# Performance work log

Measured on AMD Instinct MI355X. Metric: run time of the kernel, lower is better.

## Reference

```python
import jax, jax.numpy as jnp
import numpy as np


def setup_inputs() -> dict:
    key = jax.random.key(0)
    k1, k2, k3, k4, k5 = jax.random.split(key, 5)
    b, n, L, D, m = 8, 8192, 512, 128, 16
    x = jax.random.normal(k1, (b, n, L), dtype=jnp.float32)
    # attention MLP: Linear(L->D, no bias), Tanh, Linear(D->1, no bias)
    W1 = jax.random.normal(k2, (L, D), dtype=jnp.float32) / np.sqrt(L).astype(np.float32)
    W2 = jax.random.normal(k3, (D, 1), dtype=jnp.float32) / np.sqrt(D).astype(np.float32)
    batched_image_ids = jax.random.randint(k4, (b, n), 0, m)  # which image each packed token belongs to
    key_pad_mask = jax.random.bernoulli(k5, 0.1, (b, n))      # True = padding token
    return {"x": x, "W1": W1, "W2": W2,
            "batched_image_ids": batched_image_ids,
            "key_pad_mask": key_pad_mask,
            "max_queries": 16}


def reference(x, W1, W2, batched_image_ids, key_pad_mask, max_queries):
    # Attention scores per token: tanh(x W1) W2 -> [b, n, 1]
    A = jnp.tanh(x @ W1) @ W2
    A = jnp.swapaxes(A, -1, -2)  # [b, 1, n]
    b, n, d = x.shape
    # Per-image pooling mask: token j contributes to query i iff its image id == i and not padded
    image_id_arange = jnp.arange(max_queries)                                    # [m]
    attn_pool_mask = (image_id_arange[None, :, None] == batched_image_ids[:, None, :])
    attn_pool_mask = attn_pool_mask & (~key_pad_mask)[:, None, :]                # [b, m, n]
    neg = -jnp.finfo(A.dtype).max
    A = jnp.where(attn_pool_mask, jnp.broadcast_to(A, (b, max_queries, n)), neg)
    A = jax.nn.softmax(A, axis=-1)                                               # [b, m, n]
    out = jnp.einsum('bmn,bnd->bmd', A, x)                                       # pooled per image
    # num_images == max_queries for every bag -> is_images selects everything
    out = out.reshape(b * max_queries, d)
    return out
```

## Files before the change

### kernel.cpp

```cpp
#include <hip/hip_runtime.h>
#include <hip/hip_bf16.h>
#include <cstdint>
#include <cstddef>

typedef __attribute__((ext_vector_type(8))) short bf16x8;
typedef __attribute__((ext_vector_type(4))) float f32x4;

#define BATCH 8
#define NTOK 8192
#define LDIM 512
#define DDIM 128
#define NQ 16

static __device__ __forceinline__ short f2bf(float f) {
  uint32_t u = __float_as_uint(f);
  uint32_t r = u + 0x7fffu + ((u >> 16) & 1u);
  return (short)(r >> 16);
}

static __device__ __forceinline__ bf16x8 cvt8(float4 a, float4 b) {
  union { uint32_t u[4]; bf16x8 v; } r;
  asm("v_cvt_pk_bf16_f32 %0, %1, %2" : "=v"(r.u[0]) : "v"(a.x), "v"(a.y));
  asm("v_cvt_pk_bf16_f32 %0, %1, %2" : "=v"(r.u[1]) : "v"(a.z), "v"(a.w));
  asm("v_cvt_pk_bf16_f32 %0, %1, %2" : "=v"(r.u[2]) : "v"(b.x), "v"(b.y));
  asm("v_cvt_pk_bf16_f32 %0, %1, %2" : "=v"(r.u[3]) : "v"(b.z), "v"(b.w));
  return r.v;
}

static __device__ __forceinline__ uint32_t cvt2(float a, float b) {
  uint32_t o;
  asm("v_cvt_pk_bf16_f32 %0, %1, %2" : "=v"(o) : "v"(a), "v"(b));
  return o;
}

static __device__ __forceinline__ bool is_pad(const void* pad, int byteFlag, int j) {
  return byteFlag ? (((const unsigned char*)pad)[j] != 0)
                  : (((const int*)pad)[j] != 0);
}

__global__ __launch_bounds__(256) void k0_wfrag(const float* __restrict__ W1,
                                                short* __restrict__ wfrag,
                                                const unsigned int* __restrict__ pad_raw,
                                                int* __restrict__ flag) {
  int tid = blockIdx.x * blockDim.x + threadIdx.x;
  if (tid < 16 * 8 * 64) {
    int l = tid & 63;
    int t = (tid >> 6) & 7;
    int c = tid >> 9;
    int kbase = c * 32 + (l >> 4) * 8;
    int col = t * 16 + (l & 15);
    bf16x8 frag;
#pragma unroll
    for (int i = 0; i < 8; ++i) frag[i] = f2bf(W1[(size_t)(kbase + i) * DDIM + col]);
    ((bf16x8*)wfrag)[tid] = frag;
  }
  if (blockIdx.x == 0) {
    int any_gt1 = 0;
    for (int i = threadIdx.x; i < 16384; i += 256)
      if (pad_raw[i] > 1u) any_gt1 = 1;
    unsigned long long m = __ballot(any_gt1);
    __shared__ int s[4];
    if ((threadIdx.x & 63) == 0) s[threadIdx.x >> 6] = (m != 0ull) ? 1 : 0;
    __syncthreads();
    if (threadIdx.x == 0) flag[0] = (s[0] | s[1] | s[2] | s[3]);
  }
}

__global__ __launch_bounds__(256, 2) void k1_fused(const float* __restrict__ x,
                                                   const short* __restrict__ wfrag,
                                                   const float* __restrict__ W2,
                                                   const int* __restrict__ ids,
                                                   const void* __restrict__ pad,
                                                   const int* __restrict__ flag,
                                                   unsigned int* __restrict__ partial_bf,
                                                   float* __restrict__ wsum_p) {
  __shared__ __align__(16) char smem[81920];
  char* slab = smem;
  short* ldsW = (short*)(smem + 65536);
  float* wt_l = (float*)(smem + 65536);
  int* qq_l = (int*)(smem + 65536 + 256);
  int* idx_l = (int*)(smem + 65536 + 512);
  int* off_l = (int*)(smem + 65536 + 768);

  const int tid = threadIdx.x, wave = tid >> 6, lane = tid & 63;
  const int g = lane >> 4;
  const int row = wave * 16 + (lane & 15);
  const int rowB = blockIdx.x * 64;
  const float* xp = x + (size_t)(rowB + row) * LDIM + g * 8;
  const int swz = (row & 7) << 4;

#define STAGE_W(c, wb)                                                                        \
  {                                                                                           \
    const unsigned int* srcw_ = (const unsigned int*)wfrag + (c) * 2048;                      \
    _Pragma("unroll")                                                                         \
    for (int i = 0; i < 2; ++i) {                                                             \
      int off_ = i * 256 + tid;                                                               \
      __builtin_amdgcn_global_load_lds(                                                       \
          (const __attribute__((address_space(1))) unsigned int*)(srcw_ + off_ * 4),          \
          (__attribute__((address_space(3))) unsigned int*)&ldsW[(wb) * 4096 + off_ * 8],     \
          16, 0, 0);                                                                          \
    }                                                                                         \
  }

#define ALOAD(dst, c)                              \
  {                                                \
    dst[0] = *(const float4*)(xp + (c) * 32);      \
    dst[1] = *(const float4*)(xp + (c) * 32 + 4);  \
  }

  f32x4 acc[8];
#pragma unroll
  for (int t = 0; t < 8; ++t) acc[t] = (f32x4){0.f, 0.f, 0.f, 0.f};
  float4 avbuf[2][2];

  STAGE_W(0, 0);
  ALOAD(avbuf[0], 0);
  __syncthreads();

#pragma unroll
  for (int c = 0; c < 16; ++c) {
    if (c < 15) {
      STAGE_W(c + 1, (c + 1) & 1);
      ALOAD(avbuf[(c + 1) & 1], c + 1);
    }
    bf16x8 af = cvt8(avbuf[c & 1][0], avbuf[c & 1][1]);
    *(bf16x8*)(slab + (((row << 10) + c * 64 + g * 16) ^ swz)) = af;
#pragma unroll
    for (int t = 0; t < 8; ++t) {
      bf16x8 bfr = *(const bf16x8*)&ldsW[(c & 1) * 4096 + (t * 64 + lane) * 8];
      acc[t] = __builtin_amdgcn_mfma_f32_16x16x32_bf16(af, bfr, acc[t], 0, 0, 0);
    }
    __syncthreads();
  }
#undef STAGE_W
#undef ALOAD

  float w2v[8];
#pragma unroll
  for (int t = 0; t < 8; ++t) w2v[t] = W2[t * 16 + (lane & 15)];
  float asum[4] = {0.f, 0.f, 0.f, 0.f};
#pragma unroll
  for (int t = 0; t < 8; ++t) {
#pragma unroll
    for (int r = 0; r < 4; ++r) {
      float h = 1.f - 2.f / (__expf(2.f * acc[t][r]) + 1.f);
      asum[r] += h * w2v[t];
    }
  }
#pragma unroll
  for (int m = 1; m < 16; m <<= 1) {
#pragma unroll
    for (int r = 0; r < 4; ++r) asum[r] += __shfl_xor(asum[r], m, 64);
  }
  const int bfl = flag[0];
  if ((lane & 15) == 0) {
#pragma unroll
    for (int r = 0; r < 4; ++r) {
      int lr = wave * 16 + g * 4 + r;
      int grow = rowB + lr;
      wt_l[lr] = __expf(asum[r]);
      qq_l[lr] = is_pad(pad, bfl, grow) ? 16 : ids[grow];
    }
  }
  __syncthreads();

  if (tid < 64) {
    int q0 = qq_l[tid];
    unsigned long long below = (1ull << tid) - 1ull;
    int pos = 0;
    for (int q = 0; q < 16; ++q) {
      if (tid == 0) off_l[q] = pos;
      unsigned long long m = __ballot(q0 == q);
      if (q0 == q) idx_l[pos + __popcll(m & below)] = tid;
      pos += __popcll(m);
    }
    if (tid == 0) off_l[16] = pos;
  }
  __syncthreads();

  if (tid < 16) {
    float s = 0.f;
    for (int e = off_l[tid]; e < off_l[tid + 1]; ++e) s += wt_l[idx_l[e]];
    wsum_p[blockIdx.x * 16 + tid] = s;
  }

  const int colb = tid * 4;
#pragma unroll 1
  for (int q = 0; q < 16; ++q) {
    int e0 = off_l[q], e1 = off_l[q + 1];
    float ax = 0.f, ay = 0.f;
    for (int e = e0; e < e1; ++e) {
      int r = idx_l[e];
      uint32_t u = *(const uint32_t*)(slab + (((r << 10) + colb) ^ ((r & 7) << 4)));
      float lo = __uint_as_float(u << 16);
      float hi = __uint_as_float(u & 0xffff0000u);
      float wt = wt_l[r];
      ax = fmaf(wt, lo, ax);
      ay = fmaf(wt, hi, ay);
    }
    partial_bf[(size_t)(blockIdx.x * 16 + q) * 256 + tid] = cvt2(ax, ay);
  }
}

__global__ __launch_bounds__(256) void k4_reduce(const unsigned int* __restrict__ partial_bf,
                                                 const float* __restrict__ wsum_p,
                                                 float* __restrict__ out) {
  int b = blockIdx.x >> 4, q = blockIdx.x & 15;
  int tid = threadIdx.x;
  float ws = 0.f;
#pragma unroll 8
  for (int t = 0; t < 128; ++t) ws += wsum_p[(b * 128 + t) * 16 + q];
  float px = 0.f, py = 0.f;
#pragma unroll 4
  for (int t = 0; t < 128; ++t) {
    uint32_t u = partial_bf[(size_t)((b * 128 + t) * 16 + q) * 256 + tid];
    px += __uint_as_float(u << 16);
    py += __uint_as_float(u & 0xffff0000u);
  }
  float inv = (ws > 0.f) ? (1.f / ws) : 0.f;
  float2 o = {px * inv, py * inv};
  ((float2*)out)[(size_t)(b * 16 + q) * 256 + tid] = o;
}

extern "C" void kernel_launch(void* const* d_in, const int* in_sizes, int n_in,
                              void* d_out, int out_size, void* d_ws, size_t ws_size,
                              hipStream_t stream) {
  const float* x = (const float*)d_in[0];
  const float* W1 = (const float*)d_in[1];
  const float* W2 = (const float*)d_in[2];
  const int* ids = (const int*)d_in[3];
  const void* pad = d_in[4];
  float* out = (float*)d_out;

  char* ws = (char*)d_ws;
  short* wfrag = (short*)ws;
  int* flag = (int*)(ws + 131072);
  float* wsum_p = (float*)(ws + 131328);
  unsigned int* partial_bf = (unsigned int*)(ws + 196864);

  hipLaunchKernelGGL(k0_wfrag, dim3(32), dim3(256), 0, stream,
                     W1, wfrag, (const unsigned int*)pad, flag);
  hipLaunchKernelGGL(k1_fused, dim3((BATCH * NTOK) / 64), dim3(256), 0, stream,
                     x, wfrag, W2, ids, pad, flag, partial_bf, wsum_p);
  hipLaunchKernelGGL(k4_reduce, dim3(BATCH * NQ), dim3(256), 0, stream,
                     partial_bf, wsum_p, out);
}
```

Measured before the change: 80.92 us.

## Load W1 fragments directly into registers and deepen x prefetch

The GEMM loop no longer stages W1 fragments through LDS with async global-to-LDS copies and per-chunk barriers. Each wave now reads its W1 fragments straight from global memory (L2-resident) into double-buffered registers. x loads are prefetched four chunks ahead instead of one. This drops 16 __syncthreads and the LDS traffic for the weights. In exchange every wave issues its own redundant global W1 loads and register pressure rises, which may reduce occupancy under launch_bounds(256,2).

```diff
diff --git a/kernel.cpp b/kernel.cpp
--- a/kernel.cpp
+++ b/kernel.cpp
@@ -74,33 +74,19 @@
                                                    const int* __restrict__ flag,
                                                    unsigned int* __restrict__ partial_bf,
                                                    float* __restrict__ wsum_p) {
-  __shared__ __align__(16) char smem[81920];
-  char* slab = smem;
-  short* ldsW = (short*)(smem + 65536);
-  float* wt_l = (float*)(smem + 65536);
-  int* qq_l = (int*)(smem + 65536 + 256);
-  int* idx_l = (int*)(smem + 65536 + 512);
-  int* off_l = (int*)(smem + 65536 + 768);
+  __shared__ __align__(16) char slab[65536];
+  __shared__ float wt_l[64];
+  __shared__ int qq_l[64];
+  __shared__ int idx_l[64];
+  __shared__ int off_l[17];
 
   const int tid = threadIdx.x, wave = tid >> 6, lane = tid & 63;
   const int g = lane >> 4;
   const int row = wave * 16 + (lane & 15);
   const int rowB = blockIdx.x * 64;
   const float* xp = x + (size_t)(rowB + row) * LDIM + g * 8;
+  const bf16x8* wfp = (const bf16x8*)wfrag + lane;
   const int swz = (row & 7) << 4;
-
-#define STAGE_W(c, wb)                                                                        \
-  {                                                                                           \
-    const unsigned int* srcw_ = (const unsigned int*)wfrag + (c) * 2048;                      \
-    _Pragma("unroll")                                                                         \
-    for (int i = 0; i < 2; ++i) {                                                             \
-      int off_ = i * 256 + tid;                                                               \
-      __builtin_amdgcn_global_load_lds(                                                       \
-          (const __attribute__((address_space(1))) unsigned int*)(srcw_ + off_ * 4),          \
-          (__attribute__((address_space(3))) unsigned int*)&ldsW[(wb) * 4096 + off_ * 8],     \
-          16, 0, 0);                                                                          \
-    }                                                                                         \
-  }
 
 #define ALOAD(dst, c)                              \
   {                                                \
@@ -111,28 +97,29 @@
   f32x4 acc[8];
 #pragma unroll
   for (int t = 0; t < 8; ++t) acc[t] = (f32x4){0.f, 0.f, 0.f, 0.f};
-  float4 avbuf[2][2];
-
-  STAGE_W(0, 0);
+  float4 avbuf[4][2];
+  bf16x8 wf[2][8];
+
   ALOAD(avbuf[0], 0);
-  __syncthreads();
+  ALOAD(avbuf[1], 1);
+  ALOAD(avbuf[2], 2);
+  ALOAD(avbuf[3], 3);
+#pragma unroll
+  for (int t = 0; t < 8; ++t) wf[0][t] = wfp[t * 64];
 
 #pragma unroll
   for (int c = 0; c < 16; ++c) {
+    bf16x8 af = cvt8(avbuf[c & 3][0], avbuf[c & 3][1]);
+    *(bf16x8*)(slab + (((row << 10) + c * 64 + g * 16) ^ swz)) = af;
     if (c < 15) {
-      STAGE_W(c + 1, (c + 1) & 1);
-      ALOAD(avbuf[(c + 1) & 1], c + 1);
-    }
-    bf16x8 af = cvt8(avbuf[c & 1][0], avbuf[c & 1][1]);
-    *(bf16x8*)(slab + (((row << 10) + c * 64 + g * 16) ^ swz)) = af;
-#pragma unroll
-    for (int t = 0; t < 8; ++t) {
-      bf16x8 bfr = *(const bf16x8*)&ldsW[(c & 1) * 4096 + (t * 64 + lane) * 8];
-      acc[t] = __builtin_amdgcn_mfma_f32_16x16x32_bf16(af, bfr, acc[t], 0, 0, 0);
-    }
-    __syncthreads();
-  }
-#undef STAGE_W
+#pragma unroll
+      for (int t = 0; t < 8; ++t) wf[(c + 1) & 1][t] = wfp[((c + 1) * 8 + t) * 64];
+    }
+    if (c < 12) ALOAD(avbuf[c & 3], c + 4);
+#pragma unroll
+    for (int t = 0; t < 8; ++t)
+      acc[t] = __builtin_amdgcn_mfma_f32_16x16x32_bf16(af, wf[c & 1][t], acc[t], 0, 0, 0);
+  }
 #undef ALOAD
 
   float w2v[8];
```

Result: slower. 84.48 us (+4.4%).
